# Kernel optimization log

Measured on AMD Instinct MI355X. Metric: run time of the kernel, lower is better.

The kernel has to match this reference:

```python
import jax, jax.numpy as jnp
import numpy as np

B, S, H, D, HID = 1024, 64, 32, 32, 1024
COMP = 256          # smolgen compress_size
TOK = 32            # smolgen token_compress out dim
LN_EPS = 1e-5


def _xavier(key, shape):
    fan_in, fan_out = shape[0], shape[-1]
    std = np.sqrt(2.0 / (fan_in + fan_out))
    return jax.random.normal(key, shape, dtype=jnp.float32) * std


def setup_inputs() -> dict:
    key = jax.random.key(0)
    ks = jax.random.split(key, 12)
    x = jax.random.normal(ks[0], (B, S, HID), dtype=jnp.float32)
    # attention projections (stored [in, out], no bias on qkv)
    Wq = _xavier(ks[1], (HID, H * D))
    Wk = _xavier(ks[2], (HID, H * D))
    Wv = _xavier(ks[3], (HID, H * D))
    Wo = _xavier(ks[4], (H * D, HID))
    bo = jnp.zeros((HID,), dtype=jnp.float32)
    pos_bias = jnp.zeros((H, S, S), dtype=jnp.float32)
    # smolgen params
    tc_W = _xavier(ks[5], (HID, TOK))                  # token_compress, no bias
    pc_W = _xavier(ks[6], (S * TOK, COMP))             # position_compress linear
    pc_b = jnp.zeros((COMP,), dtype=jnp.float32)
    ln_g = jnp.ones((COMP,), dtype=jnp.float32)        # LayerNorm gamma
    ln_b = jnp.zeros((COMP,), dtype=jnp.float32)       # LayerNorm beta
    hp_W = jax.vmap(lambda k: _xavier(k, (COMP, COMP)))(jax.random.split(ks[7], H))  # [H,COMP,COMP]
    hp_b = jnp.zeros((H, COMP), dtype=jnp.float32)
    alp_W = _xavier(ks[8], (COMP, S * S))              # attention_logits_proj
    alp_b = jnp.zeros((S * S,), dtype=jnp.float32)
    return dict(x=x, Wq=Wq, Wk=Wk, Wv=Wv, Wo=Wo, bo=bo, pos_bias=pos_bias,
                tc_W=tc_W, pc_W=pc_W, pc_b=pc_b, ln_g=ln_g, ln_b=ln_b,
                hp_W=hp_W, hp_b=hp_b, alp_W=alp_W, alp_b=alp_b)


def _smolgen(x, tc_W, pc_W, pc_b, ln_g, ln_b, hp_W, hp_b, alp_W, alp_b):
    b = x.shape[0]
    flat = (x @ tc_W).reshape(b, S * TOK)              # [B, 64*32]
    pv = jax.nn.relu(flat @ pc_W + pc_b)               # [B, COMP]
    mu = jnp.mean(pv, axis=-1, keepdims=True)
    var = jnp.mean(jnp.square(pv - mu), axis=-1, keepdims=True)
    pv = (pv - mu) * jax.lax.rsqrt(var + LN_EPS) * ln_g + ln_b
    # per-head projections, vectorized over heads
    hv = jnp.einsum('bc,hcd->bhd', pv, hp_W) + hp_b    # [B, H, COMP]
    logits = jnp.einsum('bhd,de->bhe', hv, alp_W) + alp_b
    return logits.reshape(b, H, S, S)


def reference(x, Wq, Wk, Wv, Wo, bo, pos_bias, tc_W, pc_W, pc_b, ln_g, ln_b,
              hp_W, hp_b, alp_W, alp_b):
    b = x.shape[0]
    scale = 1.0 / np.sqrt(D)
    q = (x @ Wq).reshape(b, S, H, D).transpose(0, 2, 1, 3)  # [B,H,S,D]
    k = (x @ Wk).reshape(b, S, H, D).transpose(0, 2, 1, 3)
    v = (x @ Wv).reshape(b, S, H, D).transpose(0, 2, 1, 3)
    scores = jnp.einsum('bhqd,bhkd->bhqk', q, k) * scale
    scores = scores + pos_bias[None]
    scores = scores + _smolgen(x, tc_W, pc_W, pc_b, ln_g, ln_b, hp_W, hp_b, alp_W, alp_b)
    attn = jax.nn.softmax(scores, axis=-1)
    out = jnp.einsum('bhqk,bhkd->bhqd', attn, v)             # [B,H,S,D]
    out = out.transpose(0, 2, 1, 3).reshape(b, S, H * D)
    return out @ Wo + bo
```

## Files before the change

kernel.cpp:

```cpp
#include <hip/hip_runtime.h>
#include <hip/hip_bf16.h>
#include <cstdint>
#include <cstddef>

typedef __attribute__((ext_vector_type(4))) float f32x4;
typedef __attribute__((ext_vector_type(8))) short short8;
typedef unsigned short u16;
typedef __attribute__((ext_vector_type(8))) unsigned short u16x8;
typedef __attribute__((ext_vector_type(4))) unsigned short u16x4;

__device__ __forceinline__ u16 f2bf(float f) {
  union { float f; unsigned u; } v; v.f = f;
  unsigned r = v.u + 0x7FFFu + ((v.u >> 16) & 1u);
  return (u16)(r >> 16);
}
__device__ __forceinline__ float bf2f(u16 h) {
  union { unsigned u; float f; } v; v.u = ((unsigned)h) << 16;
  return v.f;
}
__device__ __forceinline__ void gload16(const u16* g, const u16* l) {
  __builtin_amdgcn_global_load_lds((const __attribute__((address_space(1))) void*)g,
                                   (__attribute__((address_space(3))) void*)l, 16, 0, 0);
}
__device__ __forceinline__ void fenced_barrier() {
  __builtin_amdgcn_sched_barrier(0);
  __builtin_amdgcn_s_barrier();
  __builtin_amdgcn_sched_barrier(0);
}

__global__ __launch_bounds__(256) void prep_w2t(
    const float* __restrict__ Wq, const float* __restrict__ Wk, const float* __restrict__ Wv,
    const float* __restrict__ tc, u16* __restrict__ W2t)
{
  __shared__ float t[32][33];
  const int tx = threadIdx.x, ty = threadIdx.y;
  const int k0 = blockIdx.x * 32, n0 = blockIdx.y * 32;
  const float* src = nullptr; int col = 0, sw = 0;
  if      (n0 < 1024) { src = Wq; col = n0;        sw = 1024; }
  else if (n0 < 2048) { src = Wk; col = n0 - 1024; sw = 1024; }
  else if (n0 < 3072) { src = Wv; col = n0 - 2048; sw = 1024; }
  else if (n0 < 3104) { src = tc; col = n0 - 3072; sw = 32;   }
  if (src) {
    #pragma unroll
    for (int r = 0; r < 4; r++) {
      int k = k0 + ty + r * 8;
      t[ty + r * 8][tx] = src[(size_t)k * sw + col + tx];
    }
  }
  __syncthreads();
  #pragma unroll
  for (int r = 0; r < 4; r++) {
    int n = n0 + ty + r * 8, k = k0 + tx;
    u16 v = src ? f2bf(t[tx][ty + r * 8]) : (u16)0;
    W2t[(size_t)n * 1024 + k] = v;
  }
}

__global__ __launch_bounds__(256) void transpose_bf(
    const float* __restrict__ src, u16* __restrict__ dst, int R, int C)
{
  __shared__ float t[32][33];
  const int tx = threadIdx.x, ty = threadIdx.y;
  const size_t zoff = (size_t)blockIdx.z * R * C;
  src += zoff; dst += zoff;
  const int c0 = blockIdx.x * 32, r0 = blockIdx.y * 32;
  #pragma unroll
  for (int r = 0; r < 4; r++)
    t[ty + r * 8][tx] = src[(size_t)(r0 + ty + r * 8) * C + c0 + tx];
  __syncthreads();
  #pragma unroll
  for (int r = 0; r < 4; r++)
    dst[(size_t)(c0 + ty + r * 8) * R + r0 + tx] = f2bf(t[tx][ty + r * 8]);
}

__global__ __launch_bounds__(256) void cvt_x(const float* __restrict__ x, u16* __restrict__ A2)
{
  size_t i = (size_t)blockIdx.x * 256 + threadIdx.x;
  f32x4 v = ((const f32x4*)x)[i];
  u16x4 o;
  #pragma unroll
  for (int j = 0; j < 4; j++) o[j] = f2bf(v[j]);
  ((u16x4*)A2)[i] = o;
}

template<int MODE>
__global__ __launch_bounds__(512, 4) void gemm_p(
    const u16* __restrict__ A, const u16* __restrict__ Bt, int K,
    void* __restrict__ o0, void* __restrict__ o1, void* __restrict__ o2, void* __restrict__ o3,
    const float* __restrict__ bias0, const float* __restrict__ bias1)
{
  __shared__ __align__(16) u16 lds[3][12288];
  const int tid = threadIdx.x;
  const int wid = tid >> 6, lane = tid & 63;
  const int wm = wid >> 1, wn = wid & 1;
  const int g = lane >> 4, l15 = lane & 15;

  const int GX = gridDim.x;
  const int nwg = GX * (int)gridDim.y;
  const int lin = (int)blockIdx.y * GX + (int)blockIdx.x;
  const int swz = (lin & 7) * (nwg >> 3) + (lin >> 3);
  const int bn = swz % GX, bm = swz / GX;

  const int lR = lane >> 3;
  const int logi = (lane & 7) ^ lR;
  const int shb = logi >> 2;
  const int sg = logi & 3;

  const u16* pA0 = A + (size_t)(bm * 256 + shb * 128 + (wid * 2 + 0) * 8 + lR) * K + sg * 8;
  const u16* pA1 = A + (size_t)(bm * 256 + shb * 128 + (wid * 2 + 1) * 8 + lR) * K + sg * 8;
  const u16* pB  = Bt + (size_t)(bn * 128 + shb * 64 + wid * 8 + lR) * K + sg * 8;

  const int aRd = ((wm & 1) * 64 + l15) * 64 + ((((wm >> 1) << 2) | g) ^ (l15 & 7)) * 8;
  const int bRd = 8192 + l15 * 64 + ((((wn << 2) | g) ^ (l15 & 7)) * 8);

  f32x4 acc[4][4];
  #pragma unroll
  for (int i = 0; i < 4; i++)
    #pragma unroll
    for (int j = 0; j < 4; j++)
      #pragma unroll
      for (int r = 0; r < 4; r++) acc[i][j][r] = 0.f;

  const int NT = K >> 5;

#define STG(buf, kt) do {                                                   \
    gload16(pA0 + (size_t)(kt) * 32, &lds[buf][(wid * 2 + 0) * 512]);       \
    gload16(pA1 + (size_t)(kt) * 32, &lds[buf][(wid * 2 + 1) * 512]);       \
    gload16(pB  + (size_t)(kt) * 32, &lds[buf][8192 + wid * 512]); } while (0)

  STG(0, 0); STG(1, 1);

  for (int t = 0; t < NT; t++) {
    const int rb = t % 3;
    const int wb = (t + 2) % 3;
    const bool more = (t + 2) < NT;

    if (t + 1 < NT) asm volatile("s_waitcnt vmcnt(3)" ::: "memory");
    else            asm volatile("s_waitcnt vmcnt(0)" ::: "memory");
    fenced_barrier();

    short8 af[4], bfr[4];
    #pragma unroll
    for (int f = 0; f < 4; f++) af[f] = *(const short8*)&lds[rb][aRd + f * 1024];
    #pragma unroll
    for (int n = 0; n < 4; n++) bfr[n] = *(const short8*)&lds[rb][bRd + n * 1024];
    if (more) STG(wb, t + 2);
    asm volatile("s_waitcnt lgkmcnt(0)" ::: "memory");
    __builtin_amdgcn_sched_barrier(0);
    __builtin_amdgcn_s_setprio(1);
    #pragma unroll
    for (int f = 0; f < 4; f++)
      #pragma unroll
      for (int n = 0; n < 4; n++)
        acc[f][n] = __builtin_amdgcn_mfma_f32_16x16x32_bf16(af[f], bfr[n], acc[f][n], 0, 0, 0);
    __builtin_amdgcn_s_setprio(0);
  }
#undef STG

  const int lr = lane >> 4, lc = lane & 15;
  #pragma unroll
  for (int fm = 0; fm < 4; fm++) {
    #pragma unroll
    for (int fn = 0; fn < 4; fn++) {
      #pragma unroll
      for (int r = 0; r < 4; r++) {
        int gm = bm * 256 + wm * 64 + fm * 16 + lr * 4 + r;
        int gn = bn * 128 + wn * 64 + fn * 16 + lc;
        float val = acc[fm][fn][r];
        if (MODE == 0) {
          int b = gm >> 6, s = gm & 63;
          if (gn < 3072) {
            int which = gn >> 10, hh = (gn >> 5) & 31, d = gn & 31;
            u16* dst = (which == 0) ? (u16*)o0 : (which == 1) ? (u16*)o1 : (u16*)o2;
            dst[(((size_t)b * 32 + hh) * 64 + s) * 32 + d] = f2bf(val);
          } else if (gn < 3104) {
            ((u16*)o3)[(size_t)b * 2048 + s * 32 + (gn - 3072)] = f2bf(val);
          }
        } else if (MODE == 3) {
          ((u16*)o0)[(size_t)gm * 4096 + gn] = f2bf(val + bias0[gn] + bias1[(gm & 31) * 4096 + gn]);
        } else {
          ((float*)o0)[(size_t)gm * 1024 + gn] = val + bias0[gn];
        }
      }
    }
  }
}

template<int MODE>
__global__ __launch_bounds__(256) void gemm_bt(
    const u16* __restrict__ A, const u16* __restrict__ Bt, int K,
    void* __restrict__ o0, const float* __restrict__ bias0)
{
  __shared__ __align__(16) u16 lA[128 * 32];
  __shared__ __align__(16) u16 lB[128 * 32];
  const int tid = threadIdx.x;
  const int wid = tid >> 6, lane = tid & 63;
  const int wm = wid >> 1, wn = wid & 1;
  const int bn = blockIdx.x, bm = blockIdx.y;
  if (MODE == 2) Bt += (size_t)blockIdx.z * 256 * 256;

  f32x4 acc[4][4];
  #pragma unroll
  for (int i = 0; i < 4; i++)
    #pragma unroll
    for (int j = 0; j < 4; j++)
      #pragma unroll
      for (int r = 0; r < 4; r++) acc[i][j][r] = 0.f;

  const u16* Arow = A + (size_t)(bm * 128) * K;
  const u16* Brow = Bt + (size_t)(bn * 128) * K;

  for (int k0 = 0; k0 < K; k0 += 32) {
    #pragma unroll
    for (int i = 0; i < 2; i++) {
      int c = wid * 128 + i * 64 + lane;
      int row = c >> 2, col = (c & 3) * 8;
      gload16(Arow + (size_t)row * K + k0 + col, &lA[(wid * 128 + i * 64) * 8]);
      gload16(Brow + (size_t)row * K + k0 + col, &lB[(wid * 128 + i * 64) * 8]);
    }
    __syncthreads();
    short8 af[4], bfr[4];
    #pragma unroll
    for (int f = 0; f < 4; f++) {
      af[f]  = *(const short8*)&lA[(wm * 64 + f * 16 + (lane & 15)) * 32 + (lane >> 4) * 8];
      bfr[f] = *(const short8*)&lB[(wn * 64 + f * 16 + (lane & 15)) * 32 + (lane >> 4) * 8];
    }
    #pragma unroll
    for (int fm = 0; fm < 4; fm++)
      #pragma unroll
      for (int fn = 0; fn < 4; fn++)
        acc[fm][fn] = __builtin_amdgcn_mfma_f32_16x16x32_bf16(af[fm], bfr[fn], acc[fm][fn], 0, 0, 0);
    __syncthreads();
  }

  const int lr = lane >> 4, lc = lane & 15;
  #pragma unroll
  for (int fm = 0; fm < 4; fm++) {
    #pragma unroll
    for (int fn = 0; fn < 4; fn++) {
      #pragma unroll
      for (int r = 0; r < 4; r++) {
        int gm = bm * 128 + wm * 64 + fm * 16 + lr * 4 + r;
        int gn = bn * 128 + wn * 64 + fn * 16 + lc;
        float val = acc[fm][fn][r];
        if (MODE == 1) {
          float v = val + bias0[gn];
          ((float*)o0)[(size_t)gm * 256 + gn] = v > 0.f ? v : 0.f;
        } else if (MODE == 2) {
          int h = blockIdx.z;
          ((u16*)o0)[((size_t)gm * 32 + h) * 256 + gn] = f2bf(val + bias0[h * 256 + gn]);
        }
      }
    }
  }
}

__global__ __launch_bounds__(256) void ln_kernel(
    const float* __restrict__ pv, const float* __restrict__ g, const float* __restrict__ b2,
    u16* __restrict__ out)
{
  __shared__ float red[256];
  const int bi = blockIdx.x, t = threadIdx.x;
  float v = pv[(size_t)bi * 256 + t];
  red[t] = v; __syncthreads();
  #pragma unroll
  for (int o = 128; o > 0; o >>= 1) { if (t < o) red[t] += red[t + o]; __syncthreads(); }
  float mu = red[0] * (1.f / 256.f);
  __syncthreads();
  float dv = v - mu;
  red[t] = dv * dv; __syncthreads();
  #pragma unroll
  for (int o = 128; o > 0; o >>= 1) { if (t < o) red[t] += red[t + o]; __syncthreads(); }
  float var = red[0] * (1.f / 256.f);
  float rs = rsqrtf(var + 1e-5f);
  out[(size_t)bi * 256 + t] = f2bf(dv * rs * g[t] + b2[t]);
}

__global__ __launch_bounds__(64) void attn_mfma(
    const u16* __restrict__ qb, const u16* __restrict__ kb, const u16* __restrict__ vb,
    const u16* __restrict__ lg, u16* __restrict__ aout)
{
  __shared__ __align__(16) u16 vT[32 * 64];
  __shared__ __align__(16) u16 Pl[64 * 64];
  const int bid = blockIdx.x;
  const int lane = threadIdx.x;
  const int g = lane >> 4, l15 = lane & 15;
  const size_t base = (size_t)bid * 2048;

  {
    const u16* vrow = vb + base + lane * 32;
    u16x8 vv[4];
    #pragma unroll
    for (int c = 0; c < 4; c++) vv[c] = *(const u16x8*)(vrow + c * 8);
    #pragma unroll
    for (int d = 0; d < 32; d++)
      vT[d * 64 + (lane ^ ((d & 7) << 3))] = vv[d >> 3][d & 7];
  }

  short8 qf[4], kf[4];
  #pragma unroll
  for (int t = 0; t < 4; t++) {
    qf[t] = *(const short8*)(qb + base + (size_t)(t * 16 + l15) * 32 + g * 8);
    kf[t] = *(const short8*)(kb + base + (size_t)(t * 16 + l15) * 32 + g * 8);
  }

  f32x4 s[4][4];
  #pragma unroll
  for (int tm = 0; tm < 4; tm++)
    #pragma unroll
    for (int tn = 0; tn < 4; tn++)
      #pragma unroll
      for (int r = 0; r < 4; r++) s[tm][tn][r] = 0.f;
  #pragma unroll
  for (int tm = 0; tm < 4; tm++)
    #pragma unroll
    for (int tn = 0; tn < 4; tn++)
      s[tm][tn] = __builtin_amdgcn_mfma_f32_16x16x32_bf16(kf[tm], qf[tn], s[tm][tn], 0, 0, 0);

  const float scale = 0.17677669529663687f;
  float inv4[4];
  const u16* lbase = lg + (size_t)bid * 4096;
  #pragma unroll
  for (int tn = 0; tn < 4; tn++) {
    const int q = tn * 16 + l15;
    float mx = -1e30f;
    #pragma unroll
    for (int tm = 0; tm < 4; tm++) {
      u16x4 u = *(const u16x4*)(lbase + (size_t)q * 64 + tm * 16 + g * 4);
      #pragma unroll
      for (int r = 0; r < 4; r++) {
        s[tm][tn][r] = s[tm][tn][r] * scale + bf2f(u[r]);
        mx = fmaxf(mx, s[tm][tn][r]);
      }
    }
    mx = fmaxf(mx, __shfl_xor(mx, 16));
    mx = fmaxf(mx, __shfl_xor(mx, 32));
    float sm = 0.f;
    #pragma unroll
    for (int tm = 0; tm < 4; tm++)
      #pragma unroll
      for (int r = 0; r < 4; r++) {
        float e = __expf(s[tm][tn][r] - mx);
        s[tm][tn][r] = e;
        sm += e;
      }
    sm += __shfl_xor(sm, 16);
    sm += __shfl_xor(sm, 32);
    inv4[tn] = 1.f / sm;
    #pragma unroll
    for (int tm = 0; tm < 4; tm++) {
      u16x4 p;
      #pragma unroll
      for (int r = 0; r < 4; r++) p[r] = f2bf(s[tm][tn][r]);
      *(u16x4*)&Pl[q * 64 + ((tm * 16 + g * 4) ^ ((q & 7) << 3))] = p;
    }
  }
  __syncthreads();

  f32x4 o[2][4];
  #pragma unroll
  for (int md = 0; md < 2; md++)
    #pragma unroll
    for (int tn = 0; tn < 4; tn++)
      #pragma unroll
      for (int r = 0; r < 4; r++) o[md][tn][r] = 0.f;
  #pragma unroll
  for (int ks = 0; ks < 2; ks++) {
    short8 vf2[2], pf[4];
    #pragma unroll
    for (int md = 0; md < 2; md++)
      vf2[md] = *(const short8*)&vT[(md * 16 + l15) * 64 + ((ks * 32 + g * 8) ^ ((l15 & 7) << 3))];
    #pragma unroll
    for (int tn = 0; tn < 4; tn++)
      pf[tn] = *(const short8*)&Pl[(tn * 16 + l15) * 64 + ((ks * 32 + g * 8) ^ ((l15 & 7) << 3))];
    #pragma unroll
    for (int md = 0; md < 2; md++)
      #pragma unroll
      for (int tn = 0; tn < 4; tn++)
        o[md][tn] = __builtin_amdgcn_mfma_f32_16x16x32_bf16(vf2[md], pf[tn], o[md][tn], 0, 0, 0);
  }

  const int b = bid >> 5, h = bid & 31;
  #pragma unroll
  for (int md = 0; md < 2; md++) {
    #pragma unroll
    for (int tn = 0; tn < 4; tn++) {
      const int q = tn * 16 + l15, d0 = md * 16 + g * 4;
      u16x4 u;
      #pragma unroll
      for (int r = 0; r < 4; r++) u[r] = f2bf(o[md][tn][r] * inv4[tn]);
      *(u16x4*)(aout + ((size_t)(b * 64 + q)) * 1024 + h * 32 + d0) = u;
    }
  }
}

extern "C" void kernel_launch(void* const* d_in, const int* in_sizes, int n_in,
                              void* d_out, int out_size, void* d_ws, size_t ws_size,
                              hipStream_t stream) {
  const float* x       = (const float*)d_in[0];
  const float* Wq      = (const float*)d_in[1];
  const float* Wk      = (const float*)d_in[2];
  const float* Wv      = (const float*)d_in[3];
  const float* Wo      = (const float*)d_in[4];
  const float* bo      = (const float*)d_in[5];
  const float* pos_b   = (const float*)d_in[6];
  const float* tc_W    = (const float*)d_in[7];
  const float* pc_W    = (const float*)d_in[8];
  const float* pc_b    = (const float*)d_in[9];
  const float* ln_g    = (const float*)d_in[10];
  const float* ln_b    = (const float*)d_in[11];
  const float* hp_W    = (const float*)d_in[12];
  const float* hp_b    = (const float*)d_in[13];
  const float* alp_W   = (const float*)d_in[14];
  const float* alp_b   = (const float*)d_in[15];
  float* out = (float*)d_out;

  char* w = (char*)d_ws;
  u16* A2     = (u16*)w;
  u16* logits = (u16*)w;              w += 268435456;
  u16* qb     = (u16*)w;              w += 134217728;
  u16* kb     = (u16*)w;              w += 134217728;
  u16* vb     = (u16*)w;              w += 134217728;
  u16* aout   = (u16*)w;              w += 134217728;
  u16* W2t    = (u16*)w;              w += (size_t)3328 * 1024 * 2;
  u16* pcWt   = (u16*)w;              w += (size_t)256 * 2048 * 2;
  u16* hpWt   = (u16*)w;              w += (size_t)32 * 256 * 256 * 2;
  u16* alpWt  = (u16*)w;              w += (size_t)4096 * 256 * 2;
  u16* WoT    = (u16*)w;              w += (size_t)1024 * 1024 * 2;
  u16* flatb  = (u16*)w;              w += (size_t)1024 * 2048 * 2;
  float* pvtmp= (float*)w;            w += (size_t)1024 * 256 * 4;
  u16* pvb    = (u16*)w;              w += (size_t)1024 * 256 * 2;
  u16* hvb    = (u16*)w;              w += (size_t)32768 * 256 * 2;

  prep_w2t    <<<dim3(32, 104),    dim3(32, 8), 0, stream>>>(Wq, Wk, Wv, tc_W, W2t);
  transpose_bf<<<dim3(8, 64, 1),   dim3(32, 8), 0, stream>>>(pc_W, pcWt, 2048, 256);
  transpose_bf<<<dim3(8, 8, 32),   dim3(32, 8), 0, stream>>>(hp_W, hpWt, 256, 256);
  transpose_bf<<<dim3(128, 8, 1),  dim3(32, 8), 0, stream>>>(alp_W, alpWt, 256, 4096);
  transpose_bf<<<dim3(32, 32, 1),  dim3(32, 8), 0, stream>>>(Wo, WoT, 1024, 1024);
  cvt_x       <<<65536, 256, 0, stream>>>(x, A2);

  gemm_p<0> <<<dim3(26, 256),    512, 0, stream>>>(A2, W2t, 1024, qb, kb, vb, flatb, nullptr, nullptr);
  gemm_bt<1><<<dim3(2, 8),       256, 0, stream>>>(flatb, pcWt, 2048, pvtmp, pc_b);
  ln_kernel <<<1024, 256, 0, stream>>>(pvtmp, ln_g, ln_b, pvb);
  gemm_bt<2><<<dim3(2, 8, 32),   256, 0, stream>>>(pvb, hpWt, 256, hvb, hp_b);
  gemm_p<3> <<<dim3(32, 128),    512, 0, stream>>>(hvb, alpWt, 256, logits, nullptr, nullptr, nullptr, alp_b, pos_b);
  attn_mfma <<<32768, 64, 0, stream>>>(qb, kb, vb, logits, aout);
  gemm_p<4> <<<dim3(8, 256),     512, 0, stream>>>(aout, WoT, 1024, out, nullptr, nullptr, nullptr, bo, nullptr);
}
```

Baseline: 1.089 ms.

## Switch gemm_p to 32x32x16 MFMA and trim padded QKV weight columns

Measured after the change: 1.135 ms. 4.2% more time.

```diff
diff --git a/kernel.cpp b/kernel.cpp
--- a/kernel.cpp
+++ b/kernel.cpp
@@ -4,6 +4,7 @@
 #include <cstddef>
 
 typedef __attribute__((ext_vector_type(4))) float f32x4;
+typedef __attribute__((ext_vector_type(16))) float f32x16;
 typedef __attribute__((ext_vector_type(8))) short short8;
 typedef unsigned short u16;
 typedef __attribute__((ext_vector_type(8))) unsigned short u16x8;
@@ -93,7 +94,7 @@
   const int tid = threadIdx.x;
   const int wid = tid >> 6, lane = tid & 63;
   const int wm = wid >> 1, wn = wid & 1;
-  const int g = lane >> 4, l15 = lane & 15;
+  const int l31 = lane & 31, l7 = lane & 7, lh = lane >> 5;
 
   const int GX = gridDim.x;
   const int nwg = GX * (int)gridDim.y;
@@ -110,16 +111,27 @@
   const u16* pA1 = A + (size_t)(bm * 256 + shb * 128 + (wid * 2 + 1) * 8 + lR) * K + sg * 8;
   const u16* pB  = Bt + (size_t)(bn * 128 + shb * 64 + wid * 8 + lR) * K + sg * 8;
 
-  const int aRd = ((wm & 1) * 64 + l15) * 64 + ((((wm >> 1) << 2) | g) ^ (l15 & 7)) * 8;
-  const int bRd = 8192 + l15 * 64 + ((((wn << 2) | g) ^ (l15 & 7)) * 8);
-
-  f32x4 acc[4][4];
-  #pragma unroll
-  for (int i = 0; i < 4; i++)
-    #pragma unroll
-    for (int j = 0; j < 4; j++)
-      #pragma unroll
-      for (int r = 0; r < 4; r++) acc[i][j][r] = 0.f;
+  int aOff[2][2], bOff[2][2];
+  #pragma unroll
+  for (int fm = 0; fm < 2; fm++)
+    #pragma unroll
+    for (int ks = 0; ks < 2; ks++)
+      aOff[fm][ks] = ((wm & 1) * 64 + fm * 32 + l31) * 64 +
+                     (((((wm >> 1) << 2) | (ks << 1) | lh) ^ l7) << 3);
+  #pragma unroll
+  for (int fj = 0; fj < 2; fj++)
+    #pragma unroll
+    for (int ks = 0; ks < 2; ks++)
+      bOff[fj][ks] = 8192 + (fj * 32 + l31) * 64 +
+                     ((((wn << 2) | (ks << 1) | lh) ^ l7) << 3);
+
+  f32x16 acc[2][2];
+  #pragma unroll
+  for (int i = 0; i < 2; i++)
+    #pragma unroll
+    for (int j = 0; j < 2; j++)
+      #pragma unroll
+      for (int r = 0; r < 16; r++) acc[i][j][r] = 0.f;
 
   const int NT = K >> 5;
 
@@ -139,34 +151,40 @@
     else            asm volatile("s_waitcnt vmcnt(0)" ::: "memory");
     fenced_barrier();
 
-    short8 af[4], bfr[4];
-    #pragma unroll
-    for (int f = 0; f < 4; f++) af[f] = *(const short8*)&lds[rb][aRd + f * 1024];
-    #pragma unroll
-    for (int n = 0; n < 4; n++) bfr[n] = *(const short8*)&lds[rb][bRd + n * 1024];
+    short8 af[2][2], bf[2][2];
+    #pragma unroll
+    for (int fm = 0; fm < 2; fm++)
+      #pragma unroll
+      for (int ks = 0; ks < 2; ks++) af[fm][ks] = *(const short8*)&lds[rb][aOff[fm][ks]];
+    #pragma unroll
+    for (int fj = 0; fj < 2; fj++)
+      #pragma unroll
+      for (int ks = 0; ks < 2; ks++) bf[fj][ks] = *(const short8*)&lds[rb][bOff[fj][ks]];
     if (more) STG(wb, t + 2);
     asm volatile("s_waitcnt lgkmcnt(0)" ::: "memory");
     __builtin_amdgcn_sched_barrier(0);
     __builtin_amdgcn_s_setprio(1);
     #pragma unroll
-    for (int f = 0; f < 4; f++)
-      #pragma unroll
-      for (int n = 0; n < 4; n++)
-        acc[f][n] = __builtin_amdgcn_mfma_f32_16x16x32_bf16(af[f], bfr[n], acc[f][n], 0, 0, 0);
+    for (int fm = 0; fm < 2; fm++)
+      #pragma unroll
+      for (int fj = 0; fj < 2; fj++)
+        #pragma unroll
+        for (int ks = 0; ks < 2; ks++)
+          acc[fm][fj] = __builtin_amdgcn_mfma_f32_32x32x16_bf16(
+              af[fm][ks], bf[fj][ks], acc[fm][fj], 0, 0, 0);
     __builtin_amdgcn_s_setprio(0);
   }
 #undef STG
 
-  const int lr = lane >> 4, lc = lane & 15;
-  #pragma unroll
-  for (int fm = 0; fm < 4; fm++) {
-    #pragma unroll
-    for (int fn = 0; fn < 4; fn++) {
-      #pragma unroll
-      for (int r = 0; r < 4; r++) {
-        int gm = bm * 256 + wm * 64 + fm * 16 + lr * 4 + r;
-        int gn = bn * 128 + wn * 64 + fn * 16 + lc;
-        float val = acc[fm][fn][r];
+  #pragma unroll
+  for (int fi = 0; fi < 2; fi++) {
+    #pragma unroll
+    for (int fj = 0; fj < 2; fj++) {
+      #pragma unroll
+      for (int r = 0; r < 16; r++) {
+        int gm = bm * 256 + wm * 64 + fi * 32 + (r & 3) + 8 * (r >> 2) + 4 * lh;
+        int gn = bn * 128 + wn * 64 + fj * 32 + l31;
+        float val = acc[fi][fj][r];
         if (MODE == 0) {
           int b = gm >> 6, s = gm & 63;
           if (gn < 3072) {
@@ -422,7 +440,7 @@
   u16* kb     = (u16*)w;              w += 134217728;
   u16* vb     = (u16*)w;              w += 134217728;
   u16* aout   = (u16*)w;              w += 134217728;
-  u16* W2t    = (u16*)w;              w += (size_t)3328 * 1024 * 2;
+  u16* W2t    = (u16*)w;              w += (size_t)3200 * 1024 * 2;
   u16* pcWt   = (u16*)w;              w += (size_t)256 * 2048 * 2;
   u16* hpWt   = (u16*)w;              w += (size_t)32 * 256 * 256 * 2;
   u16* alpWt  = (u16*)w;              w += (size_t)4096 * 256 * 2;
@@ -432,14 +450,14 @@
   u16* pvb    = (u16*)w;              w += (size_t)1024 * 256 * 2;
   u16* hvb    = (u16*)w;              w += (size_t)32768 * 256 * 2;
 
-  prep_w2t    <<<dim3(32, 104),    dim3(32, 8), 0, stream>>>(Wq, Wk, Wv, tc_W, W2t);
+  prep_w2t    <<<dim3(32, 100),    dim3(32, 8), 0, stream>>>(Wq, Wk, Wv, tc_W, W2t);
   transpose_bf<<<dim3(8, 64, 1),   dim3(32, 8), 0, stream>>>(pc_W, pcWt, 2048, 256);
   transpose_bf<<<dim3(8, 8, 32),   dim3(32, 8), 0, stream>>>(hp_W, hpWt, 256, 256);
   transpose_bf<<<dim3(128, 8, 1),  dim3(32, 8), 0, stream>>>(alp_W, alpWt, 256, 4096);
   transpose_bf<<<dim3(32, 32, 1),  dim3(32, 8), 0, stream>>>(Wo, WoT, 1024, 1024);
   cvt_x       <<<65536, 256, 0, stream>>>(x, A2);
 
-  gemm_p<0> <<<dim3(26, 256),    512, 0, stream>>>(A2, W2t, 1024, qb, kb, vb, flatb, nullptr, nullptr);
+  gemm_p<0> <<<dim3(25, 256),    512, 0, stream>>>(A2, W2t, 1024, qb, kb, vb, flatb, nullptr, nullptr);
   gemm_bt<1><<<dim3(2, 8),       256, 0, stream>>>(flatb, pcWt, 2048, pvtmp, pc_b);
   ln_kernel <<<1024, 256, 0, stream>>>(pvtmp, ln_g, ln_b, pvb);
   gemm_bt<2><<<dim3(2, 8, 32),   256, 0, stream>>>(pvb, hpWt, 256, hvb, hp_b);
```
